# Performance work log

Hardware: AMD Instinct MI355X
Metric: run time of the kernel (lower is better)

Reference implementation:

```python
import jax, jax.numpy as jnp
import numpy as np

B, S, H, NH = 2, 2048, 2048, 16
HD = H // NH  # 128


def setup_inputs() -> dict:
    key = jax.random.key(0)
    ks = jax.random.split(key, 6)
    x = jax.random.normal(ks[0], (B, S, H), dtype=jnp.float32)
    # causal additive mask: 0 on/below diagonal, -1e9 above
    causal = jnp.triu(jnp.full((S, S), -1e9, dtype=jnp.float32), k=1)
    attention_mask = causal[None, None, :, :]  # [1,1,S,S]
    # ALiBi: per-head slope * key position, broadcast over queries
    slopes = 2.0 ** (-8.0 * (jnp.arange(NH, dtype=jnp.float32) + 1) / NH)
    alibi = (-slopes[:, None] * jnp.arange(S, dtype=jnp.float32)[None, :])
    alibi = alibi[None, :, None, :]  # [1,NH,1,S]
    scale = 0.02
    Wq = jax.random.normal(ks[1], (H, H), dtype=jnp.float32) * scale
    Wk = jax.random.normal(ks[2], (H, H), dtype=jnp.float32) * scale
    Wv = jax.random.normal(ks[3], (H, H), dtype=jnp.float32) * scale
    Wo = jax.random.normal(ks[4], (H, H), dtype=jnp.float32) * scale
    return {"x": x, "attention_mask": attention_mask, "alibi": alibi,
            "Wq": Wq, "Wk": Wk, "Wv": Wv, "Wo": Wo}


def reference(x, attention_mask, alibi, Wq, Wk, Wv, Wo):
    b, s, _ = x.shape
    # nn.Linear(y) = y @ W.T
    q = (x @ Wq.T).reshape(b, s, NH, HD).transpose(0, 2, 1, 3)  # [b,h,s,d]
    k = (x @ Wk.T).reshape(b, s, NH, HD).transpose(0, 2, 1, 3)
    v = (x @ Wv.T).reshape(b, s, NH, HD).transpose(0, 2, 1, 3)
    scores = jnp.einsum('bhqd,bhkd->bhqk', q, k) / jnp.sqrt(jnp.float32(HD))
    scores = scores + alibi + attention_mask
    attn = jax.nn.softmax(scores, axis=-1)
    out = jnp.einsum('bhqk,bhkd->bhqd', attn, v)
    out = out.transpose(0, 2, 1, 3).reshape(b, s, H)
    return out @ Wo.T
```

## Files before the change

### kernel.cpp

```cpp
#include <hip/hip_runtime.h>

typedef unsigned short u16;
typedef float f32x4 __attribute__((ext_vector_type(4)));
typedef short s16x8 __attribute__((ext_vector_type(8)));
typedef short s16x4 __attribute__((ext_vector_type(4)));
typedef unsigned short u16x4 __attribute__((ext_vector_type(4)));

#define S_LEN 2048
#define HDIM 2048
#define NHEADS 16
#define HEAD_DIM 128

__device__ __forceinline__ u16 f2bf(float f) {
    unsigned u = __builtin_bit_cast(unsigned, f);
    u += 0x7FFFu + ((u >> 16) & 1u);
    return (u16)(u >> 16);
}

__device__ __forceinline__ void gload_lds16(const u16* g, u16* l) {
    __builtin_amdgcn_global_load_lds(
        (const __attribute__((address_space(1))) unsigned int*)(const void*)g,
        (__attribute__((address_space(3))) unsigned int*)(void*)l, 16, 0, 0);
}

__device__ __forceinline__ void tr_read16(const u16* bptr, s16x4* o) {
    auto p = (const __attribute__((address_space(3))) u16*)(const void*)bptr;
    asm volatile(
        "ds_read_b64_tr_b16 %0, %16\n\t"
        "ds_read_b64_tr_b16 %1, %16 offset:1024\n\t"
        "ds_read_b64_tr_b16 %2, %16 offset:128\n\t"
        "ds_read_b64_tr_b16 %3, %16 offset:1152\n\t"
        "ds_read_b64_tr_b16 %4, %16 offset:256\n\t"
        "ds_read_b64_tr_b16 %5, %16 offset:1280\n\t"
        "ds_read_b64_tr_b16 %6, %16 offset:384\n\t"
        "ds_read_b64_tr_b16 %7, %16 offset:1408\n\t"
        "ds_read_b64_tr_b16 %8, %16 offset:512\n\t"
        "ds_read_b64_tr_b16 %9, %16 offset:1536\n\t"
        "ds_read_b64_tr_b16 %10, %16 offset:640\n\t"
        "ds_read_b64_tr_b16 %11, %16 offset:1664\n\t"
        "ds_read_b64_tr_b16 %12, %16 offset:768\n\t"
        "ds_read_b64_tr_b16 %13, %16 offset:1792\n\t"
        "ds_read_b64_tr_b16 %14, %16 offset:896\n\t"
        "ds_read_b64_tr_b16 %15, %16 offset:1920\n\t"
        "s_waitcnt lgkmcnt(0)"
        : "=&v"(o[0]), "=&v"(o[1]), "=&v"(o[2]), "=&v"(o[3]),
          "=&v"(o[4]), "=&v"(o[5]), "=&v"(o[6]), "=&v"(o[7]),
          "=&v"(o[8]), "=&v"(o[9]), "=&v"(o[10]), "=&v"(o[11]),
          "=&v"(o[12]), "=&v"(o[13]), "=&v"(o[14]), "=&v"(o[15])
        : "v"(p));
    __builtin_amdgcn_sched_barrier(0);
}

__global__ void cvt_bf16(const float* __restrict__ in, u16* __restrict__ out, int n4, float scale) {
    int i = blockIdx.x * blockDim.x + threadIdx.x;
    int stride = gridDim.x * blockDim.x;
    for (; i < n4; i += stride) {
        float4 f = ((const float4*)in)[i];
        u16x4 r;
        r.x = f2bf(f.x * scale); r.y = f2bf(f.y * scale);
        r.z = f2bf(f.z * scale); r.w = f2bf(f.w * scale);
        *(u16x4*)(out + (size_t)i * 4) = r;
    }
}

__global__ void cvt_w4(const float* __restrict__ w0, const float* __restrict__ w1,
                       const float* __restrict__ w2, const float* __restrict__ w3,
                       u16* __restrict__ out, float scale0) {
    const int n4each = (HDIM * HDIM) / 4;
    int b = blockIdx.x;
    int which = b >> 11;
    const float* src = which == 0 ? w0 : which == 1 ? w1 : which == 2 ? w2 : w3;
    float sc = which == 0 ? scale0 : 1.0f;
    u16* dst = out + (size_t)which * (HDIM * HDIM);
    int i = (b & 2047) * 256 + threadIdx.x;
    const int stride = 2048 * 256;
    for (; i < n4each; i += stride) {
        float4 f = ((const float4*)src)[i];
        u16x4 r;
        r.x = f2bf(f.x * sc); r.y = f2bf(f.y * sc);
        r.z = f2bf(f.z * sc); r.w = f2bf(f.w * sc);
        *(u16x4*)(dst + (size_t)i * 4) = r;
    }
}

#define PBAR __builtin_amdgcn_s_barrier()
#define SGB0 __builtin_amdgcn_sched_barrier(0)
#define LGKM0 { asm volatile("s_waitcnt lgkmcnt(0)" ::: "memory"); SGB0; }

template<int OUT_F32>
__global__ __launch_bounds__(512, 2) void gemm_128x256(const u16* __restrict__ A, const u16* __restrict__ Bw,
                                                       void* __restrict__ C0, void* __restrict__ C1,
                                                       void* __restrict__ C2, int M, int N, int K) {
    __shared__ u16 lA[2][128 * 64];
    __shared__ u16 lB[2][256 * 64];

    int bid = blockIdx.x;
    const int nwg = gridDim.x;
    bid = (bid & 7) * (nwg >> 3) + (bid >> 3);

    const int nbn = N >> 8;
    const int bm = bid / nbn, bn = bid % nbn;
    const int t = threadIdx.x, lane = t & 63, w = t >> 6;
    const int wm = w >> 2, wn = w & 3;
    const int rqg = lane >> 4, rl = lane & 15;

    const size_t rowA0 = (size_t)bm * 128;
    const int colB0 = bn << 8;

    const u16* srcA[2]; int dA[2];
#pragma unroll
    for (int i = 0; i < 2; ++i) {
        int c = t + i * 512;
        int row = c >> 3, ch = c & 7;
        srcA[i] = A + (rowA0 + row) * (size_t)K + ((ch ^ (row & 7)) << 3);
        dA[i] = c * 8;
    }
    const u16* srcB[4]; int dB[4];
#pragma unroll
    for (int i = 0; i < 4; ++i) {
        int c = t + i * 512;
        int row = c >> 3, ch = c & 7;
        srcB[i] = Bw + (size_t)(colB0 + row) * (size_t)K + ((ch ^ (row & 7)) << 3);
        dB[i] = c * 8;
    }

    auto stA = [&](int side, int tile) {
        const size_t go = (size_t)tile * 64;
#pragma unroll
        for (int i = 0; i < 2; ++i) gload_lds16(srcA[i] + go, &lA[side][dA[i]]);
    };
    auto stB = [&](int side, int tile) {
        const size_t go = (size_t)tile * 64;
#pragma unroll
        for (int i = 0; i < 4; ++i) gload_lds16(srcB[i] + go, &lB[side][dB[i]]);
    };

    const int chv[2] = { ((0 + rqg) ^ (rl & 7)) << 3, ((4 + rqg) ^ (rl & 7)) << 3 };
    const int arow = wm * 64, brow = wn * 64;

    f32x4 acc[4][4] = {};
    s16x8 af[4][2], bfL[2][2], bfH[2][2];

    auto ldA = [&](const u16* sAp) {
#pragma unroll
        for (int m = 0; m < 4; ++m)
#pragma unroll
            for (int k = 0; k < 2; ++k)
                af[m][k] = *(const s16x8*)&sAp[(arow + m * 16 + rl) * 64 + chv[k]];
    };
    auto ldB = [&](s16x8 (&bf)[2][2], const u16* sBp, int half) {
#pragma unroll
        for (int n = 0; n < 2; ++n)
#pragma unroll
            for (int k = 0; k < 2; ++k)
                bf[n][k] = *(const s16x8*)&sBp[(brow + half * 32 + n * 16 + rl) * 64 + chv[k]];
    };
    auto mm = [&](s16x8 (&bf)[2][2], int half) {
        __builtin_amdgcn_s_setprio(1);
#pragma unroll
        for (int m = 0; m < 4; ++m)
#pragma unroll
            for (int n = 0; n < 2; ++n)
#pragma unroll
                for (int k = 0; k < 2; ++k)
                    acc[m][half * 2 + n] = __builtin_amdgcn_mfma_f32_16x16x32_bf16(
                        af[m][k], bf[n][k], acc[m][half * 2 + n], 0, 0, 0);
        __builtin_amdgcn_s_setprio(0);
    };

    const int NT = K >> 6;
    const int NI = NT >> 1;

    stA(0, 0); stB(0, 0); stA(1, 1); stB(1, 1);
    asm volatile("s_waitcnt vmcnt(6)" ::: "memory");
    PBAR;

    for (int j = 0; j < NI; ++j) {
        const bool more2 = (2 * j + 2 < NT);
        const bool more3 = (2 * j + 3 < NT);

        ldA(lA[0]); ldB(bfL, lB[0], 0);
        if (j > 0) stB(1, 2 * j + 1);
        PBAR; LGKM0;
        mm(bfL, 0);
        PBAR;
        ldB(bfH, lB[0], 1);
        if (more2) stA(0, 2 * j + 2);
        PBAR; LGKM0;
        mm(bfH, 1);
        if (more2) { asm volatile("s_waitcnt vmcnt(2)" ::: "memory"); }
        else       { asm volatile("s_waitcnt vmcnt(0)" ::: "memory"); }
        PBAR;
        ldA(lA[1]); ldB(bfL, lB[1], 0);
        if (more2) stB(0, 2 * j + 2);
        PBAR; LGKM0;
        mm(bfL, 0);
        PBAR;
        ldB(bfH, lB[1], 1);
        if (more3) stA(1, 2 * j + 3);
        PBAR; LGKM0;
        mm(bfH, 1);
        if (more3) { asm volatile("s_waitcnt vmcnt(2)" ::: "memory"); }
        else       { asm volatile("s_waitcnt vmcnt(0)" ::: "memory"); }
        PBAR;
    }

    const int mat = colB0 >> 11;
    void* Csel = mat == 0 ? C0 : mat == 1 ? C1 : C2;
    const int colb = (colB0 & 2047) + wn * 64;
#pragma unroll
    for (int m = 0; m < 4; ++m) {
#pragma unroll
        for (int n = 0; n < 4; ++n) {
#pragma unroll
            for (int j = 0; j < 4; ++j) {
                size_t row = rowA0 + wm * 64 + m * 16 + rqg * 4 + j;
                size_t col = colb + n * 16 + rl;
                float v = acc[m][n][j];
                if (OUT_F32) ((float*)Csel)[row * 2048 + col] = v;
                else ((u16*)Csel)[row * 2048 + col] = f2bf(v);
            }
        }
    }
}

__global__ __launch_bounds__(512) void attn_kernel(const u16* __restrict__ Q, const u16* __restrict__ Kb,
                                                   const u16* __restrict__ Vb,
                                                   const float* __restrict__ alibi,
                                                   u16* __restrict__ O) {
    __shared__ u16 lK[2][64 * 128];
    __shared__ u16 lV[2][64 * 128];
    __shared__ u16 lP[8][16 * 80];

    const int bid = blockIdx.x;
    const int bh = bid & 31;
    const int p = bid >> 5;
    const int h = bh & 15, b = bh >> 4;
    const int t = threadIdx.x, lane = t & 63, w = t >> 6;
    const int rqg = lane >> 4, rl = lane & 15;

    const size_t bS = (size_t)b * S_LEN;
    const size_t hOff = (size_t)h * HEAD_DIM;

    const u16* ksrc[2]; const u16* vsrc[2]; int cdst[2];
#pragma unroll
    for (int i = 0; i < 2; ++i) {
        int c = t + i * 512;
        int krow = c >> 4, kch = c & 15;
        ksrc[i] = Kb + (bS + krow) * HDIM + hOff + ((kch ^ (krow & 7)) << 3);
        int vkey = ((c >> 6) << 2) + ((c >> 1) & 3);
        int vd = (((c >> 3) & 7) << 4) + ((c & 1) << 3);
        vsrc[i] = Vb + (bS + vkey) * HDIM + hOff + vd;
        cdst[i] = c * 8;
    }

    const float mslope2 = alibi[(size_t)h * S_LEN + 1] * 1.4426950408889634f;

    s16x8 ones;
#pragma unroll
    for (int i = 0; i < 8; ++i) ones[i] = (short)0x3F80;

    for (int sidx = 0; sidx < 2; ++sidx) {
        const int qt = sidx ? (15 - p) : p;
        const int q0w = qt * 128 + w * 16;

        const size_t baseQ = (bS + q0w + rl) * HDIM + hOff;
        s16x8 qf[4];
#pragma unroll
        for (int kk = 0; kk < 4; ++kk)
            qf[kk] = *(const s16x8*)(Q + baseQ + kk * 32 + rqg * 8);

        float m[4];
        f32x4 o[8]; f32x4 osum = {0.f, 0.f, 0.f, 0.f};
#pragma unroll
        for (int j = 0; j < 4; ++j) m[j] = -1e30f;
#pragma unroll
        for (int n = 0; n < 8; ++n) o[n] = (f32x4){0.f, 0.f, 0.f, 0.f};

        const int nkt = 2 * qt + 2;
        const int my_last = 2 * qt + (w >> 2);
        u16* lPw = lP[w];

#pragma unroll
        for (int i = 0; i < 2; ++i) {
            gload_lds16(ksrc[i], &lK[0][cdst[i]]);
            gload_lds16(vsrc[i], &lV[0][cdst[i]]);
        }
        __syncthreads();

        for (int kt = 0; kt < nkt; ++kt) {
            const int cur = kt & 1;
            if (kt + 1 < nkt) {
                const size_t goff = (size_t)(kt + 1) * 64 * HDIM;
#pragma unroll
                for (int i = 0; i < 2; ++i) {
                    gload_lds16(ksrc[i] + goff, &lK[cur ^ 1][cdst[i]]);
                    gload_lds16(vsrc[i] + goff, &lV[cur ^ 1][cdst[i]]);
                }
            }

            if (kt <= my_last) {
                const int k0 = kt * 64;

                f32x4 sfr[4] = {};
#pragma unroll
                for (int kk = 0; kk < 4; ++kk) {
#pragma unroll
                    for (int nt = 0; nt < 4; ++nt) {
                        int row = nt * 16 + rl;
                        int off = row * 256 + ((kk * 64 + rqg * 16) ^ ((row & 7) << 4));
                        s16x8 kf = *(const s16x8*)((const char*)lK[cur] + off);
                        sfr[nt] = __builtin_amdgcn_mfma_f32_16x16x32_bf16(qf[kk], kf, sfr[nt], 0, 0, 0);
                    }
                }

                const bool diag = (kt == my_last);
                float scv[4][4];
                float thr0 = m[0] + 8.f, thr1 = m[1] + 8.f, thr2 = m[2] + 8.f, thr3 = m[3] + 8.f;
                int small = 1;
#pragma unroll
                for (int nt = 0; nt < 4; ++nt) {
                    int key = k0 + nt * 16 + rl;
                    float al = mslope2 * (float)key;
#pragma unroll
                    for (int j = 0; j < 4; ++j) {
                        float v = sfr[nt][j] + al;
                        if (diag) {
                            int qrow = q0w + rqg * 4 + j;
                            v = (key <= qrow) ? v : -1e30f;
                        }
                        scv[nt][j] = v;
                        float thr = (j == 0) ? thr0 : (j == 1) ? thr1 : (j == 2) ? thr2 : thr3;
                        small &= (v <= thr) ? 1 : 0;
                    }
                }
                if (!__all(small)) {
                    float rmax[4];
#pragma unroll
                    for (int j = 0; j < 4; ++j)
                        rmax[j] = fmaxf(fmaxf(scv[0][j], scv[1][j]), fmaxf(scv[2][j], scv[3][j]));
#pragma unroll
                    for (int off = 1; off < 16; off <<= 1) {
#pragma unroll
                        for (int j = 0; j < 4; ++j) rmax[j] = fmaxf(rmax[j], __shfl_xor(rmax[j], off));
                    }
#pragma unroll
                    for (int j = 0; j < 4; ++j) {
                        float mn = fmaxf(m[j], rmax[j]);
                        float fac = exp2f(m[j] - mn);
                        m[j] = mn;
                        osum[j] *= fac;
#pragma unroll
                        for (int n = 0; n < 8; ++n) o[n][j] *= fac;
                    }
                }

#pragma unroll
                for (int nt = 0; nt < 4; ++nt) {
#pragma unroll
                    for (int j = 0; j < 4; ++j) {
                        float pv = exp2f(scv[nt][j] - m[j]);
                        lPw[(rqg * 4 + j) * 80 + nt * 16 + rl] = f2bf(pv);
                    }
                }

                const u16* lVbase = &lV[cur][0] + rqg * 1024 + rl * 4;
#pragma unroll
                for (int kk = 0; kk < 2; ++kk) {
                    s16x8 pf = *(const s16x8*)&lPw[rl * 80 + kk * 32 + rqg * 8];
                    osum = __builtin_amdgcn_mfma_f32_16x16x32_bf16(pf, ones, osum, 0, 0, 0);
                    s16x4 tr[16];
                    tr_read16(lVbase + kk * 4096, tr);
#pragma unroll
                    for (int n = 0; n < 8; ++n) {
                        s16x8 vf = __builtin_shufflevector(tr[2 * n], tr[2 * n + 1], 0, 1, 2, 3, 4, 5, 6, 7);
                        o[n] = __builtin_amdgcn_mfma_f32_16x16x32_bf16(pf, vf, o[n], 0, 0, 0);
                    }
                }
            }
            __syncthreads();
        }

        float inv[4];
#pragma unroll
        for (int j = 0; j < 4; ++j) inv[j] = 1.0f / osum[j];
#pragma unroll
        for (int n = 0; n < 8; ++n) {
#pragma unroll
            for (int j = 0; j < 4; ++j) {
                size_t row = bS + q0w + rqg * 4 + j;
                O[row * HDIM + hOff + n * 16 + rl] = f2bf(o[n][j] * inv[j]);
            }
        }
    }
}

extern "C" void kernel_launch(void* const* d_in, const int* in_sizes, int n_in,
                              void* d_out, int out_size, void* d_ws, size_t ws_size,
                              hipStream_t stream) {
    (void)in_sizes; (void)n_in; (void)out_size; (void)ws_size;
    const float* x     = (const float*)d_in[0];
    const float* alibi = (const float*)d_in[2];
    const float* Wq    = (const float*)d_in[3];
    const float* Wk    = (const float*)d_in[4];
    const float* Wv    = (const float*)d_in[5];
    const float* Wo    = (const float*)d_in[6];
    float* out = (float*)d_out;

    char* ws = (char*)d_ws;
    u16* xb  = (u16*)(ws + 0);
    u16* wqb = (u16*)(ws + 16777216);
    u16* Qb  = (u16*)(ws + 50331648);
    u16* Kv  = Qb + 8388608;
    u16* Vv  = Kv + 8388608;
    u16* Ob  = Vv + 8388608;
    u16* wob = wqb + 3 * 4194304;

    const int M = 2 * S_LEN;
    const int K = HDIM;

    const float qscale = 0.08838834764831845f * 1.4426950408889634f;
    cvt_bf16<<<4096, 256, 0, stream>>>(x, xb, (2 * S_LEN * HDIM) / 4, 1.0f);
    cvt_w4<<<8192, 256, 0, stream>>>(Wq, Wk, Wv, Wo, wqb, qscale);

    gemm_128x256<0><<<(M / 128) * (3 * HDIM / 256), 512, 0, stream>>>(xb, wqb, Qb, Kv, Vv, M, 3 * HDIM, K);

    attn_kernel<<<2 * NHEADS * 8, 512, 0, stream>>>(Qb, Kv, Vv, alibi, Ob);

    gemm_128x256<1><<<(M / 128) * (HDIM / 256), 512, 0, stream>>>(Ob, wob, out, out, out, M, HDIM, K);
}
```

Measured before the change: 267.6 us.

## Use triple-buffered LDS ring with one barrier per tile in GEMM and attention

Replaces the double-buffered, half-tile-split GEMM main loop with a 3-stage LDS ring. Each K tile now loads all A/B fragments at once, prefetches two tiles ahead, and uses a single barrier per tile instead of four. The attention kernel gets the same 3-stage K/V ring, with vmcnt waits and s_barrier in place of __syncthreads. The GEMM block-to-tile mapping is also changed to group tiles per XCD for better L2 locality. The trade-offs are more LDS (about 147KB for the GEMM) and more live B-fragment registers, which could hurt scheduling.

```diff
diff --git a/kernel.cpp b/kernel.cpp
--- a/kernel.cpp
+++ b/kernel.cpp
@@ -22,6 +22,9 @@
         (const __attribute__((address_space(1))) unsigned int*)(const void*)g,
         (__attribute__((address_space(3))) unsigned int*)(void*)l, 16, 0, 0);
 }
+
+#define PBAR __builtin_amdgcn_s_barrier()
+#define SGB0 __builtin_amdgcn_sched_barrier(0)
 
 __device__ __forceinline__ void tr_read16(const u16* bptr, s16x4* o) {
     auto p = (const __attribute__((address_space(3))) u16*)(const void*)bptr;
@@ -83,23 +86,19 @@
     }
 }
 
-#define PBAR __builtin_amdgcn_s_barrier()
-#define SGB0 __builtin_amdgcn_sched_barrier(0)
-#define LGKM0 { asm volatile("s_waitcnt lgkmcnt(0)" ::: "memory"); SGB0; }
-
 template<int OUT_F32>
-__global__ __launch_bounds__(512, 2) void gemm_128x256(const u16* __restrict__ A, const u16* __restrict__ Bw,
-                                                       void* __restrict__ C0, void* __restrict__ C1,
-                                                       void* __restrict__ C2, int M, int N, int K) {
-    __shared__ u16 lA[2][128 * 64];
-    __shared__ u16 lB[2][256 * 64];
-
-    int bid = blockIdx.x;
-    const int nwg = gridDim.x;
-    bid = (bid & 7) * (nwg >> 3) + (bid >> 3);
-
-    const int nbn = N >> 8;
-    const int bm = bid / nbn, bn = bid % nbn;
+__global__ __launch_bounds__(512, 2) void gemm_ring(const u16* __restrict__ A, const u16* __restrict__ Bw,
+                                                    void* __restrict__ C0, void* __restrict__ C1,
+                                                    void* __restrict__ C2, int M, int N, int K) {
+    __shared__ u16 lds[3 * 24576];
+
+    const int bid = blockIdx.x;
+    const int xcd = bid & 7;
+    const int q = bid >> 3;
+    const int rr = q & 31, sc0 = q >> 5;
+    const int bm = xcd * 4 + (rr & 3);
+    const int bn = sc0 * 8 + (rr >> 2);
+
     const int t = threadIdx.x, lane = t & 63, w = t >> 6;
     const int wm = w >> 2, wn = w & 3;
     const int rqg = lane >> 4, rl = lane & 15;
@@ -124,85 +123,61 @@
         dB[i] = c * 8;
     }
 
-    auto stA = [&](int side, int tile) {
+    auto stage = [&](int tile, int s) {
         const size_t go = (size_t)tile * 64;
-#pragma unroll
-        for (int i = 0; i < 2; ++i) gload_lds16(srcA[i] + go, &lA[side][dA[i]]);
-    };
-    auto stB = [&](int side, int tile) {
-        const size_t go = (size_t)tile * 64;
-#pragma unroll
-        for (int i = 0; i < 4; ++i) gload_lds16(srcB[i] + go, &lB[side][dB[i]]);
+        u16* base = &lds[s * 24576];
+#pragma unroll
+        for (int i = 0; i < 2; ++i) gload_lds16(srcA[i] + go, base + dA[i]);
+#pragma unroll
+        for (int i = 0; i < 4; ++i) gload_lds16(srcB[i] + go, base + 8192 + dB[i]);
     };
 
     const int chv[2] = { ((0 + rqg) ^ (rl & 7)) << 3, ((4 + rqg) ^ (rl & 7)) << 3 };
     const int arow = wm * 64, brow = wn * 64;
 
     f32x4 acc[4][4] = {};
-    s16x8 af[4][2], bfL[2][2], bfH[2][2];
-
-    auto ldA = [&](const u16* sAp) {
-#pragma unroll
-        for (int m = 0; m < 4; ++m)
-#pragma unroll
-            for (int k = 0; k < 2; ++k)
-                af[m][k] = *(const s16x8*)&sAp[(arow + m * 16 + rl) * 64 + chv[k]];
-    };
-    auto ldB = [&](s16x8 (&bf)[2][2], const u16* sBp, int half) {
-#pragma unroll
-        for (int n = 0; n < 2; ++n)
-#pragma unroll
-            for (int k = 0; k < 2; ++k)
-                bf[n][k] = *(const s16x8*)&sBp[(brow + half * 32 + n * 16 + rl) * 64 + chv[k]];
-    };
-    auto mm = [&](s16x8 (&bf)[2][2], int half) {
-        __builtin_amdgcn_s_setprio(1);
-#pragma unroll
-        for (int m = 0; m < 4; ++m)
-#pragma unroll
-            for (int n = 0; n < 2; ++n)
-#pragma unroll
-                for (int k = 0; k < 2; ++k)
-                    acc[m][half * 2 + n] = __builtin_amdgcn_mfma_f32_16x16x32_bf16(
-                        af[m][k], bf[n][k], acc[m][half * 2 + n], 0, 0, 0);
-        __builtin_amdgcn_s_setprio(0);
-    };
 
     const int NT = K >> 6;
-    const int NI = NT >> 1;
-
-    stA(0, 0); stB(0, 0); stA(1, 1); stB(1, 1);
+
+    stage(0, 0); stage(1, 1);
     asm volatile("s_waitcnt vmcnt(6)" ::: "memory");
     PBAR;
 
-    for (int j = 0; j < NI; ++j) {
-        const bool more2 = (2 * j + 2 < NT);
-        const bool more3 = (2 * j + 3 < NT);
-
-        ldA(lA[0]); ldB(bfL, lB[0], 0);
-        if (j > 0) stB(1, 2 * j + 1);
-        PBAR; LGKM0;
-        mm(bfL, 0);
+    int s = 0;
+    for (int tt = 0; tt < NT; ++tt) {
+        const u16* sA = &lds[s * 24576];
+        const u16* sB = sA + 8192;
+
+        s16x8 af[4][2], bf[4][2];
+#pragma unroll
+        for (int m = 0; m < 4; ++m)
+#pragma unroll
+            for (int k = 0; k < 2; ++k)
+                af[m][k] = *(const s16x8*)&sA[(arow + m * 16 + rl) * 64 + chv[k]];
+#pragma unroll
+        for (int n = 0; n < 4; ++n)
+#pragma unroll
+            for (int k = 0; k < 2; ++k)
+                bf[n][k] = *(const s16x8*)&sB[(brow + n * 16 + rl) * 64 + chv[k]];
+
+        int s2 = s + 2; if (s2 >= 3) s2 -= 3;
+        if (tt + 2 < NT) stage(tt + 2, s2);
+        SGB0;
+
+        __builtin_amdgcn_s_setprio(1);
+#pragma unroll
+        for (int m = 0; m < 4; ++m)
+#pragma unroll
+            for (int n = 0; n < 4; ++n)
+#pragma unroll
+                for (int k = 0; k < 2; ++k)
+                    acc[m][n] = __builtin_amdgcn_mfma_f32_16x16x32_bf16(af[m][k], bf[n][k], acc[m][n], 0, 0, 0);
+        __builtin_amdgcn_s_setprio(0);
+
+        if (tt + 2 < NT)      { asm volatile("s_waitcnt vmcnt(6)" ::: "memory"); }
+        else if (tt + 1 < NT) { asm volatile("s_waitcnt vmcnt(0)" ::: "memory"); }
         PBAR;
-        ldB(bfH, lB[0], 1);
-        if (more2) stA(0, 2 * j + 2);
-        PBAR; LGKM0;
-        mm(bfH, 1);
-        if (more2) { asm volatile("s_waitcnt vmcnt(2)" ::: "memory"); }
-        else       { asm volatile("s_waitcnt vmcnt(0)" ::: "memory"); }
-        PBAR;
-        ldA(lA[1]); ldB(bfL, lB[1], 0);
-        if (more2) stB(0, 2 * j + 2);
-        PBAR; LGKM0;
-        mm(bfL, 0);
-        PBAR;
-        ldB(bfH, lB[1], 1);
-        if (more3) stA(1, 2 * j + 3);
-        PBAR; LGKM0;
-        mm(bfH, 1);
-        if (more3) { asm volatile("s_waitcnt vmcnt(2)" ::: "memory"); }
-        else       { asm volatile("s_waitcnt vmcnt(0)" ::: "memory"); }
-        PBAR;
+        ++s; if (s == 3) s = 0;
     }
 
     const int mat = colB0 >> 11;
@@ -228,8 +203,7 @@
                                                    const u16* __restrict__ Vb,
                                                    const float* __restrict__ alibi,
                                                    u16* __restrict__ O) {
-    __shared__ u16 lK[2][64 * 128];
-    __shared__ u16 lV[2][64 * 128];
+    __shared__ u16 ldsKV[3 * 16384];
     __shared__ u16 lP[8][16 * 80];
 
     const int bid = blockIdx.x;
@@ -254,6 +228,16 @@
         cdst[i] = c * 8;
     }
 
+    auto stageKV = [&](int tile, int s) {
+        const size_t goff = (size_t)tile * 64 * HDIM;
+        u16* base = &ldsKV[s * 16384];
+#pragma unroll
+        for (int i = 0; i < 2; ++i) {
+            gload_lds16(ksrc[i] + goff, base + cdst[i]);
+            gload_lds16(vsrc[i] + goff, base + 8192 + cdst[i]);
+        }
+    };
+
     const float mslope2 = alibi[(size_t)h * S_LEN + 1] * 1.4426950408889634f;
 
     s16x8 ones;
@@ -281,26 +265,18 @@
         const int my_last = 2 * qt + (w >> 2);
         u16* lPw = lP[w];
 
-#pragma unroll
-        for (int i = 0; i < 2; ++i) {
-            gload_lds16(ksrc[i], &lK[0][cdst[i]]);
-            gload_lds16(vsrc[i], &lV[0][cdst[i]]);
-        }
-        __syncthreads();
-
+        stageKV(0, 0); stageKV(1, 1);
+        asm volatile("s_waitcnt vmcnt(4)" ::: "memory");
+        PBAR;
+
+        int s = 0;
         for (int kt = 0; kt < nkt; ++kt) {
-            const int cur = kt & 1;
-            if (kt + 1 < nkt) {
-                const size_t goff = (size_t)(kt + 1) * 64 * HDIM;
-#pragma unroll
-                for (int i = 0; i < 2; ++i) {
-                    gload_lds16(ksrc[i] + goff, &lK[cur ^ 1][cdst[i]]);
-                    gload_lds16(vsrc[i] + goff, &lV[cur ^ 1][cdst[i]]);
-                }
-            }
+            int s2 = s + 2; if (s2 >= 3) s2 -= 3;
+            if (kt + 2 < nkt) stageKV(kt + 2, s2);
 
             if (kt <= my_last) {
                 const int k0 = kt * 64;
+                const u16* kbase = &ldsKV[s * 16384];
 
                 f32x4 sfr[4] = {};
 #pragma unroll
@@ -309,7 +285,7 @@
                     for (int nt = 0; nt < 4; ++nt) {
                         int row = nt * 16 + rl;
                         int off = row * 256 + ((kk * 64 + rqg * 16) ^ ((row & 7) << 4));
-                        s16x8 kf = *(const s16x8*)((const char*)lK[cur] + off);
+                        s16x8 kf = *(const s16x8*)((const char*)kbase + off);
                         sfr[nt] = __builtin_amdgcn_mfma_f32_16x16x32_bf16(qf[kk], kf, sfr[nt], 0, 0, 0);
                     }
                 }
@@ -364,7 +340,7 @@
                     }
                 }
 
-                const u16* lVbase = &lV[cur][0] + rqg * 1024 + rl * 4;
+                const u16* lVbase = &ldsKV[s * 16384] + 8192 + rqg * 1024 + rl * 4;
 #pragma unroll
                 for (int kk = 0; kk < 2; ++kk) {
                     s16x8 pf = *(const s16x8*)&lPw[rl * 80 + kk * 32 + rqg * 8];
@@ -378,7 +354,11 @@
                     }
                 }
             }
-            __syncthreads();
+
+            if (kt + 2 < nkt)      { asm volatile("s_waitcnt vmcnt(4)" ::: "memory"); }
+            else if (kt + 1 < nkt) { asm volatile("s_waitcnt vmcnt(0)" ::: "memory"); }
+            PBAR;
+            ++s; if (s == 3) s = 0;
         }
 
         float inv[4];
@@ -423,9 +403,9 @@
     cvt_bf16<<<4096, 256, 0, stream>>>(x, xb, (2 * S_LEN * HDIM) / 4, 1.0f);
     cvt_w4<<<8192, 256, 0, stream>>>(Wq, Wk, Wv, Wo, wqb, qscale);
 
-    gemm_128x256<0><<<(M / 128) * (3 * HDIM / 256), 512, 0, stream>>>(xb, wqb, Qb, Kv, Vv, M, 3 * HDIM, K);
+    gemm_ring<0><<<(M / 128) * (3 * HDIM / 256), 512, 0, stream>>>(xb, wqb, Qb, Kv, Vv, M, 3 * HDIM, K);
 
     attn_kernel<<<2 * NHEADS * 8, 512, 0, stream>>>(Qb, Kv, Vv, alibi, Ob);
 
-    gemm_128x256<1><<<(M / 128) * (HDIM / 256), 512, 0, stream>>>(Ob, wob, out, out, out, M, HDIM, K);
-}
+    gemm_ring<1><<<(M / 128) * (HDIM / 256), 512, 0, stream>>>(Ob, wob, out, out, out, M, HDIM, K);
+}
```

Measured after the change: 254.2 us. 1.05x faster.
